# Kernel optimization log

Hardware: AMD Instinct MI355X
Metric: run time of the kernel (lower is better)

Reference implementation:

```python
import jax, jax.numpy as jnp
import numpy as np

B, T = 32, 2048
Q_DIM, K_DIM, V_DIM, A_DIM = 512, 512, 512, 128
TEMP = 1.0


def setup_inputs() -> dict:
    key = jax.random.key(0)
    ks = jax.random.split(key, 8)
    return {
        "query": jax.random.normal(ks[0], (B, Q_DIM), dtype=jnp.float32),
        "keys": jax.random.normal(ks[1], (B, T, K_DIM), dtype=jnp.float32),
        "values": jax.random.normal(ks[2], (B, T, V_DIM), dtype=jnp.float32),
        "prev_attention_weights": jax.random.uniform(ks[3], (B, T), dtype=jnp.float32),
        "mask": jnp.ones((B, T), dtype=jnp.int32),
        # learned params (nn.Linear weight is [out,in]; store as [in,out])
        "Wq": jax.random.normal(ks[4], (Q_DIM, A_DIM), dtype=jnp.float32) * 0.02,
        "Wk": jax.random.normal(ks[5], (K_DIM, A_DIM), dtype=jnp.float32) * 0.02,
        "We": jax.random.normal(ks[6], (A_DIM, 1), dtype=jnp.float32) * 0.02,
    }


def reference(query, keys, values, prev_attention_weights, mask, Wq, Wk, We):
    # additive attention energies
    qp = query @ Wq                                   # [B, A]
    kp = jnp.einsum('btk,ka->bta', keys, Wk)          # [B, T, A]
    energy = jnp.squeeze(jnp.tanh(kp + qp[:, None, :]) @ We, -1)  # [B, T]
    energy = jnp.where(mask == 0, -jnp.inf, energy)
    raw = jax.nn.softmax(energy / TEMP, axis=1)
    # forward attention: fw[0]=raw[0]; fw[t]=(prev[t-1]+prev[t])*raw[t] for t>=1
    prev = prev_attention_weights
    prev_shift = jnp.pad(prev[:, :-1], ((0, 0), (1, 0)))  # prev[t-1], zero at t=0
    fw = raw * (prev + prev_shift)
    fw = fw.at[:, 0].set(raw[:, 0])
    fw = fw / (fw.sum(axis=1, keepdims=True) + 1e-8)
    context = jnp.einsum('bt,btd->bd', fw, values)    # [B, V_DIM]
    return context, fw
```

## Files before the change

### kernel.cpp

```cpp
#include <hip/hip_runtime.h>
#include <cstdint>
#include <cstddef>


#define T_ 2048
#define KD 512
#define AD 128

typedef __attribute__((ext_vector_type(8))) short bf16x8;
typedef __attribute__((ext_vector_type(4))) float f32x4;

__device__ __forceinline__ unsigned pack2bf(float a, float b) {
    unsigned ua = __float_as_uint(a), ub = __float_as_uint(b);
    ua += 0x7FFFu + ((ua >> 16) & 1u);
    ub += 0x7FFFu + ((ub >> 16) & 1u);
    return (ua >> 16) | (ub & 0xFFFF0000u);
}

__global__ __launch_bounds__(256) void prep_kernel(
    const float* __restrict__ query, const float* __restrict__ Wq,
    const float* __restrict__ Wk, float* __restrict__ qp,
    unsigned short* __restrict__ WkT)
{
    __shared__ float sq[128];
    const int tid = threadIdx.x;
    if (blockIdx.x < 32) {
        const int b = blockIdx.x;
        const int a = tid & 127, half = tid >> 7;
        const float* q = query + (size_t)b * KD + half * 256;
        const float* w = Wq + (size_t)(half * 256) * AD + a;
        float s0 = 0.f, s1 = 0.f, s2 = 0.f, s3 = 0.f;
        #pragma unroll 4
        for (int k = 0; k < 256; k += 4) {
            s0 += q[k + 0] * w[(size_t)(k + 0) * AD];
            s1 += q[k + 1] * w[(size_t)(k + 1) * AD];
            s2 += q[k + 2] * w[(size_t)(k + 2) * AD];
            s3 += q[k + 3] * w[(size_t)(k + 3) * AD];
        }
        float s = (s0 + s1) + (s2 + s3);
        if (half == 0) sq[a] = s;
        __syncthreads();
        if (half == 1) qp[(size_t)b * AD + a] = sq[a] + s;
    } else {
        const int blk2 = blockIdx.x - 32;
        const int n = tid & 127, kr = tid >> 7;
        #pragma unroll
        for (int kk = 0; kk < 8; kk++) {
            int k = blk2 * 16 + kr * 8 + kk;
            float v = Wk[(size_t)k * AD + n];
            unsigned u = __float_as_uint(v);
            u += 0x7FFFu + ((u >> 16) & 1u);
            WkT[(size_t)n * KD + k] = (unsigned short)(u >> 16);
        }
    }
}

__global__ __launch_bounds__(256, 2) void energy_kernel(
    const float* __restrict__ keys, const unsigned short* __restrict__ WkT,
    const float* __restrict__ qp, const float* __restrict__ We,
    float* __restrict__ energy)
{
    __shared__ __align__(16) unsigned short sA[128 * 40];
    __shared__ __align__(16) unsigned short sB[128 * 40];
    const int tid = threadIdx.x;
    const int m0 = blockIdx.x * 128;
    const int b = m0 >> 11;

    const int row = tid >> 1, half = tid & 1;
    const float* gA = keys + (size_t)(m0 + row) * KD + half * 16;
    const unsigned short* gB = WkT + (size_t)row * KD + half * 16;
    unsigned short* dA = &sA[row * 40 + half * 16];
    unsigned short* dB = &sB[row * 40 + half * 16];

    const int lane = tid & 63, wv = tid >> 6;
    const int lr = lane & 15, quad = lane >> 4;

    f32x4 acc[2][8];
    #pragma unroll
    for (int mt = 0; mt < 2; mt++)
        #pragma unroll
        for (int nt = 0; nt < 8; nt++)
            acc[mt][nt] = (f32x4){0.f, 0.f, 0.f, 0.f};

    for (int k0 = 0; k0 < KD; k0 += 32) {
        float4 f0 = *(const float4*)(gA + k0 + 0);
        float4 f1 = *(const float4*)(gA + k0 + 4);
        float4 f2 = *(const float4*)(gA + k0 + 8);
        float4 f3 = *(const float4*)(gA + k0 + 12);
        uint4 pa0, pa1;
        pa0.x = pack2bf(f0.x, f0.y); pa0.y = pack2bf(f0.z, f0.w);
        pa0.z = pack2bf(f1.x, f1.y); pa0.w = pack2bf(f1.z, f1.w);
        pa1.x = pack2bf(f2.x, f2.y); pa1.y = pack2bf(f2.z, f2.w);
        pa1.z = pack2bf(f3.x, f3.y); pa1.w = pack2bf(f3.z, f3.w);
        uint4 b0 = *(const uint4*)(gB + k0);
        uint4 b1 = *(const uint4*)(gB + k0 + 8);
        ((uint4*)dA)[0] = pa0; ((uint4*)dA)[1] = pa1;
        ((uint4*)dB)[0] = b0;  ((uint4*)dB)[1] = b1;
        __syncthreads();

        bf16x8 af[2], bfm[8];
        #pragma unroll
        for (int mt = 0; mt < 2; mt++)
            af[mt] = *(const bf16x8*)&sA[(wv * 32 + mt * 16 + lr) * 40 + quad * 8];
        #pragma unroll
        for (int nt = 0; nt < 8; nt++)
            bfm[nt] = *(const bf16x8*)&sB[(nt * 16 + lr) * 40 + quad * 8];
        #pragma unroll
        for (int mt = 0; mt < 2; mt++)
            #pragma unroll
            for (int nt = 0; nt < 8; nt++)
                acc[mt][nt] = __builtin_amdgcn_mfma_f32_16x16x32_bf16(
                    af[mt], bfm[nt], acc[mt][nt], 0, 0, 0);
        __syncthreads();
    }

    float part[2][4] = {{0.f, 0.f, 0.f, 0.f}, {0.f, 0.f, 0.f, 0.f}};
    #pragma unroll
    for (int nt = 0; nt < 8; nt++) {
        int col = nt * 16 + lr;
        float we = We[col];
        float q  = qp[(size_t)b * AD + col];
        #pragma unroll
        for (int mt = 0; mt < 2; mt++)
            #pragma unroll
            for (int r = 0; r < 4; r++) {
                float x = acc[mt][nt][r] + q;
                float e2 = __expf(2.0f * x);
                float th = 1.0f - 2.0f / (e2 + 1.0f);
                part[mt][r] += we * th;
            }
    }
    #pragma unroll
    for (int mt = 0; mt < 2; mt++)
        #pragma unroll
        for (int r = 0; r < 4; r++) {
            float v = part[mt][r];
            v += __shfl_xor(v, 1); v += __shfl_xor(v, 2);
            v += __shfl_xor(v, 4); v += __shfl_xor(v, 8);
            if (lr == 0)
                energy[(size_t)m0 + wv * 32 + mt * 16 + quad * 4 + r] = v;
        }
}

__device__ __forceinline__ float block_red_max(float v, float* sred) {
    #pragma unroll
    for (int m = 1; m < 64; m <<= 1) v = fmaxf(v, __shfl_xor(v, m));
    if ((threadIdx.x & 63) == 0) sred[threadIdx.x >> 6] = v;
    __syncthreads();
    float r = fmaxf(fmaxf(sred[0], sred[1]), fmaxf(sred[2], sred[3]));
    __syncthreads();
    return r;
}
__device__ __forceinline__ float block_red_sum(float v, float* sred) {
    #pragma unroll
    for (int m = 1; m < 64; m <<= 1) v += __shfl_xor(v, m);
    if ((threadIdx.x & 63) == 0) sred[threadIdx.x >> 6] = v;
    __syncthreads();
    float r = (sred[0] + sred[1]) + (sred[2] + sred[3]);
    __syncthreads();
    return r;
}

__global__ __launch_bounds__(256) void ctx_fused_kernel(
    const float* __restrict__ energy, const float* __restrict__ prev,
    const int* __restrict__ mask, const float* __restrict__ values,
    float* __restrict__ fw, float* __restrict__ part)
{
    __shared__ float sred[4];
    __shared__ float sfw[2048];
    __shared__ float4 sacc[128];
    const int b = blockIdx.x >> 4, ts = blockIdx.x & 15;
    const int tid = threadIdx.x;
    const size_t base = (size_t)b * T_;

    float e[8];
    #pragma unroll
    for (int i = 0; i < 8; i++) {
        int t = tid + 256 * i;
        float ev = energy[base + t];
        if (mask[base + t] == 0) ev = -__builtin_inff();
        e[i] = ev;
    }
    float mx = e[0];
    #pragma unroll
    for (int i = 1; i < 8; i++) mx = fmaxf(mx, e[i]);
    mx = block_red_max(mx, sred);

    float ex[8]; float s = 0.f;
    #pragma unroll
    for (int i = 0; i < 8; i++) { ex[i] = __expf(e[i] - mx); s += ex[i]; }
    s = block_red_sum(s, sred);
    const float invS = 1.0f / s;

    float fwv[8]; float s2 = 0.f;
    #pragma unroll
    for (int i = 0; i < 8; i++) {
        int t = tid + 256 * i;
        float pv = prev[base + t];
        float pm = (t == 0) ? 0.f : prev[base + t - 1];
        float r = ex[i] * invS;
        fwv[i] = (t == 0) ? r : r * (pv + pm);
        s2 += fwv[i];
    }
    s2 = block_red_sum(s2, sred);
    const float invD = 1.0f / (s2 + 1e-8f);
    #pragma unroll
    for (int i = 0; i < 8; i++)
        sfw[tid + 256 * i] = fwv[i] * invD;
    __syncthreads();

    const int t0 = ts * 128;
    if (tid < 128) fw[base + t0 + tid] = sfw[t0 + tid];

    const int d4 = tid & 127, tp = tid >> 7;
    const float* sf = &sfw[t0];
    const float4* vp = (const float4*)values + ((size_t)b * T_ + t0 + tp) * 128 + d4;
    float4 acc = {0.f, 0.f, 0.f, 0.f};
    #pragma unroll 8
    for (int i = 0; i < 64; i++) {
        float f = sf[tp + 2 * i];
        float4 v = vp[(size_t)i * 256];
        acc.x += f * v.x; acc.y += f * v.y; acc.z += f * v.z; acc.w += f * v.w;
    }
    if (tp) sacc[d4] = acc;
    __syncthreads();
    if (!tp) {
        float4 o = sacc[d4];
        o.x += acc.x; o.y += acc.y; o.z += acc.z; o.w += acc.w;
        ((float4*)part)[(size_t)blockIdx.x * 128 + d4] = o;
    }
}

__global__ __launch_bounds__(256) void ctx_reduce_kernel(
    const float* __restrict__ part, float* __restrict__ ctx)
{
    const int idx = blockIdx.x * 256 + threadIdx.x;
    const int b = idx >> 9, d = idx & 511;
    float s = 0.f;
    #pragma unroll
    for (int ts = 0; ts < 16; ts++)
        s += part[((size_t)(b * 16 + ts)) * 512 + d];
    ctx[idx] = s;
}

extern "C" void kernel_launch(void* const* d_in, const int* in_sizes, int n_in,
                              void* d_out, int out_size, void* d_ws, size_t ws_size,
                              hipStream_t stream) {
    const float* query  = (const float*)d_in[0];
    const float* keys   = (const float*)d_in[1];
    const float* values = (const float*)d_in[2];
    const float* prev   = (const float*)d_in[3];
    const int*   mask   = (const int*)d_in[4];
    const float* Wq     = (const float*)d_in[5];
    const float* Wk     = (const float*)d_in[6];
    const float* We     = (const float*)d_in[7];

    float* ctx = (float*)d_out;
    float* fw  = ctx + 32 * 512;

    float* wsf = (float*)d_ws;
    float* qp     = wsf;
    float* part   = wsf + 4096;
    float* energy = wsf + 4096 + 262144;
    unsigned short* WkT = (unsigned short*)(wsf + 4096 + 262144 + 65536);

    prep_kernel<<<dim3(64), dim3(256), 0, stream>>>(query, Wq, Wk, qp, WkT);
    energy_kernel<<<dim3(512), dim3(256), 0, stream>>>(keys, WkT, qp, We, energy);
    ctx_fused_kernel<<<dim3(512), dim3(256), 0, stream>>>(energy, prev, mask, values, fw, part);
    ctx_reduce_kernel<<<dim3(64), dim3(256), 0, stream>>>(part, ctx);
}
```

Baseline: 310.9 us.

## Load MFMA fragments directly from global memory and prefetch values before softmax

The energy GEMM no longer stages keys and WkT through LDS. Each wave loads its own A and B fragments straight from global memory into registers, which removes the shared-memory round trip and both block barriers per k-step. The trade-off is more redundant global/L2 reads of WkT and less coalesced key loads. The context kernel also issues the first eight value loads before the softmax reductions, overlapping their latency with that computation at the cost of extra registers.

```diff
diff --git a/kernel.cpp b/kernel.cpp
--- a/kernel.cpp
+++ b/kernel.cpp
@@ -55,25 +55,20 @@
     }
 }
 
-__global__ __launch_bounds__(256, 2) void energy_kernel(
+__global__ __launch_bounds__(256) void energy_kernel(
     const float* __restrict__ keys, const unsigned short* __restrict__ WkT,
     const float* __restrict__ qp, const float* __restrict__ We,
     float* __restrict__ energy)
 {
-    __shared__ __align__(16) unsigned short sA[128 * 40];
-    __shared__ __align__(16) unsigned short sB[128 * 40];
     const int tid = threadIdx.x;
-    const int m0 = blockIdx.x * 128;
-    const int b = m0 >> 11;
-
-    const int row = tid >> 1, half = tid & 1;
-    const float* gA = keys + (size_t)(m0 + row) * KD + half * 16;
-    const unsigned short* gB = WkT + (size_t)row * KD + half * 16;
-    unsigned short* dA = &sA[row * 40 + half * 16];
-    unsigned short* dB = &sB[row * 40 + half * 16];
-
     const int lane = tid & 63, wv = tid >> 6;
     const int lr = lane & 15, quad = lane >> 4;
+    const int m0 = blockIdx.x * 128 + wv * 32;
+    const int b = (blockIdx.x * 128) >> 11;
+
+    const float* gA0 = keys + (size_t)(m0 + lr) * KD + quad * 8;
+    const float* gA1 = keys + (size_t)(m0 + 16 + lr) * KD + quad * 8;
+    const unsigned short* gB = WkT + (size_t)lr * KD + quad * 8;
 
     f32x4 acc[2][8];
     #pragma unroll
@@ -82,36 +77,31 @@
         for (int nt = 0; nt < 8; nt++)
             acc[mt][nt] = (f32x4){0.f, 0.f, 0.f, 0.f};
 
+    #pragma unroll 2
     for (int k0 = 0; k0 < KD; k0 += 32) {
-        float4 f0 = *(const float4*)(gA + k0 + 0);
-        float4 f1 = *(const float4*)(gA + k0 + 4);
-        float4 f2 = *(const float4*)(gA + k0 + 8);
-        float4 f3 = *(const float4*)(gA + k0 + 12);
-        uint4 pa0, pa1;
-        pa0.x = pack2bf(f0.x, f0.y); pa0.y = pack2bf(f0.z, f0.w);
-        pa0.z = pack2bf(f1.x, f1.y); pa0.w = pack2bf(f1.z, f1.w);
-        pa1.x = pack2bf(f2.x, f2.y); pa1.y = pack2bf(f2.z, f2.w);
-        pa1.z = pack2bf(f3.x, f3.y); pa1.w = pack2bf(f3.z, f3.w);
-        uint4 b0 = *(const uint4*)(gB + k0);
-        uint4 b1 = *(const uint4*)(gB + k0 + 8);
-        ((uint4*)dA)[0] = pa0; ((uint4*)dA)[1] = pa1;
-        ((uint4*)dB)[0] = b0;  ((uint4*)dB)[1] = b1;
-        __syncthreads();
-
-        bf16x8 af[2], bfm[8];
-        #pragma unroll
-        for (int mt = 0; mt < 2; mt++)
-            af[mt] = *(const bf16x8*)&sA[(wv * 32 + mt * 16 + lr) * 40 + quad * 8];
+        uint4 braw[8];
         #pragma unroll
         for (int nt = 0; nt < 8; nt++)
-            bfm[nt] = *(const bf16x8*)&sB[(nt * 16 + lr) * 40 + quad * 8];
-        #pragma unroll
-        for (int mt = 0; mt < 2; mt++)
-            #pragma unroll
-            for (int nt = 0; nt < 8; nt++)
-                acc[mt][nt] = __builtin_amdgcn_mfma_f32_16x16x32_bf16(
-                    af[mt], bfm[nt], acc[mt][nt], 0, 0, 0);
-        __syncthreads();
+            braw[nt] = *(const uint4*)(gB + (size_t)(nt * 16) * KD + k0);
+        float4 a00 = *(const float4*)(gA0 + k0);
+        float4 a01 = *(const float4*)(gA0 + k0 + 4);
+        float4 a10 = *(const float4*)(gA1 + k0);
+        float4 a11 = *(const float4*)(gA1 + k0 + 4);
+        uint4 p0, p1;
+        p0.x = pack2bf(a00.x, a00.y); p0.y = pack2bf(a00.z, a00.w);
+        p0.z = pack2bf(a01.x, a01.y); p0.w = pack2bf(a01.z, a01.w);
+        p1.x = pack2bf(a10.x, a10.y); p1.y = pack2bf(a10.z, a10.w);
+        p1.z = pack2bf(a11.x, a11.y); p1.w = pack2bf(a11.z, a11.w);
+        bf16x8 af0, af1;
+        __builtin_memcpy(&af0, &p0, 16);
+        __builtin_memcpy(&af1, &p1, 16);
+        #pragma unroll
+        for (int nt = 0; nt < 8; nt++) {
+            bf16x8 bf;
+            __builtin_memcpy(&bf, &braw[nt], 16);
+            acc[0][nt] = __builtin_amdgcn_mfma_f32_16x16x32_bf16(af0, bf, acc[0][nt], 0, 0, 0);
+            acc[1][nt] = __builtin_amdgcn_mfma_f32_16x16x32_bf16(af1, bf, acc[1][nt], 0, 0, 0);
+        }
     }
 
     float part[2][4] = {{0.f, 0.f, 0.f, 0.f}, {0.f, 0.f, 0.f, 0.f}};
@@ -138,7 +128,7 @@
             v += __shfl_xor(v, 1); v += __shfl_xor(v, 2);
             v += __shfl_xor(v, 4); v += __shfl_xor(v, 8);
             if (lr == 0)
-                energy[(size_t)m0 + wv * 32 + mt * 16 + quad * 4 + r] = v;
+                energy[(size_t)m0 + mt * 16 + quad * 4 + r] = v;
         }
 }
 
@@ -172,6 +162,13 @@
     const int b = blockIdx.x >> 4, ts = blockIdx.x & 15;
     const int tid = threadIdx.x;
     const size_t base = (size_t)b * T_;
+    const int t0 = ts * 128;
+
+    const int d4 = tid & 127, tp = tid >> 7;
+    const float4* vp = (const float4*)values + ((size_t)b * T_ + t0 + tp) * 128 + d4;
+    float4 pre[8];
+    #pragma unroll
+    for (int i = 0; i < 8; i++) pre[i] = vp[(size_t)i * 256];
 
     float e[8];
     #pragma unroll
@@ -209,15 +206,18 @@
         sfw[tid + 256 * i] = fwv[i] * invD;
     __syncthreads();
 
-    const int t0 = ts * 128;
     if (tid < 128) fw[base + t0 + tid] = sfw[t0 + tid];
 
-    const int d4 = tid & 127, tp = tid >> 7;
     const float* sf = &sfw[t0];
-    const float4* vp = (const float4*)values + ((size_t)b * T_ + t0 + tp) * 128 + d4;
     float4 acc = {0.f, 0.f, 0.f, 0.f};
+    #pragma unroll
+    for (int i = 0; i < 8; i++) {
+        float f = sf[tp + 2 * i];
+        float4 v = pre[i];
+        acc.x += f * v.x; acc.y += f * v.y; acc.z += f * v.z; acc.w += f * v.w;
+    }
     #pragma unroll 8
-    for (int i = 0; i < 64; i++) {
+    for (int i = 8; i < 64; i++) {
         float f = sf[tp + 2 * i];
         float4 v = vp[(size_t)i * 256];
         acc.x += f * v.x; acc.y += f * v.y; acc.z += f * v.z; acc.w += f * v.w;
```

After: 318.6 us. 2.5% more time.

## Double-buffer LDS tiles in energy GEMM and prefetch values before softmax

Applied to the files above, without the earlier changes.

The energy kernel now uses double-buffered shared-memory tiles. Each iteration issues the global loads for the next K slice before running the MFMAs on the current slice, then converts and stores that next slice into the alternate buffer, which halves the barriers per iteration. The context kernel issues its first eight value loads at kernel entry so they overlap with the softmax and forward-attention reductions. The cost is double the LDS footprint and extra registers for the prefetched data, which may lower occupancy.

```diff
diff --git a/kernel.cpp b/kernel.cpp
--- a/kernel.cpp
+++ b/kernel.cpp
@@ -60,8 +60,8 @@
     const float* __restrict__ qp, const float* __restrict__ We,
     float* __restrict__ energy)
 {
-    __shared__ __align__(16) unsigned short sA[128 * 40];
-    __shared__ __align__(16) unsigned short sB[128 * 40];
+    __shared__ __align__(16) unsigned short sA[2][128 * 40];
+    __shared__ __align__(16) unsigned short sB[2][128 * 40];
     const int tid = threadIdx.x;
     const int m0 = blockIdx.x * 128;
     const int b = m0 >> 11;
@@ -69,8 +69,7 @@
     const int row = tid >> 1, half = tid & 1;
     const float* gA = keys + (size_t)(m0 + row) * KD + half * 16;
     const unsigned short* gB = WkT + (size_t)row * KD + half * 16;
-    unsigned short* dA = &sA[row * 40 + half * 16];
-    unsigned short* dB = &sB[row * 40 + half * 16];
+    const int doff = row * 40 + half * 16;
 
     const int lane = tid & 63, wv = tid >> 6;
     const int lr = lane & 15, quad = lane >> 4;
@@ -82,36 +81,60 @@
         for (int nt = 0; nt < 8; nt++)
             acc[mt][nt] = (f32x4){0.f, 0.f, 0.f, 0.f};
 
-    for (int k0 = 0; k0 < KD; k0 += 32) {
-        float4 f0 = *(const float4*)(gA + k0 + 0);
-        float4 f1 = *(const float4*)(gA + k0 + 4);
-        float4 f2 = *(const float4*)(gA + k0 + 8);
-        float4 f3 = *(const float4*)(gA + k0 + 12);
+    {
+        float4 f0 = *(const float4*)(gA + 0);
+        float4 f1 = *(const float4*)(gA + 4);
+        float4 f2 = *(const float4*)(gA + 8);
+        float4 f3 = *(const float4*)(gA + 12);
+        uint4 b0 = *(const uint4*)(gB + 0);
+        uint4 b1 = *(const uint4*)(gB + 8);
         uint4 pa0, pa1;
         pa0.x = pack2bf(f0.x, f0.y); pa0.y = pack2bf(f0.z, f0.w);
         pa0.z = pack2bf(f1.x, f1.y); pa0.w = pack2bf(f1.z, f1.w);
         pa1.x = pack2bf(f2.x, f2.y); pa1.y = pack2bf(f2.z, f2.w);
         pa1.z = pack2bf(f3.x, f3.y); pa1.w = pack2bf(f3.z, f3.w);
-        uint4 b0 = *(const uint4*)(gB + k0);
-        uint4 b1 = *(const uint4*)(gB + k0 + 8);
-        ((uint4*)dA)[0] = pa0; ((uint4*)dA)[1] = pa1;
-        ((uint4*)dB)[0] = b0;  ((uint4*)dB)[1] = b1;
-        __syncthreads();
-
+        ((uint4*)&sA[0][doff])[0] = pa0; ((uint4*)&sA[0][doff])[1] = pa1;
+        ((uint4*)&sB[0][doff])[0] = b0;  ((uint4*)&sB[0][doff])[1] = b1;
+    }
+    __syncthreads();
+
+    int cur = 0;
+    for (int k0 = 0; k0 < KD; k0 += 32) {
+        const int kn = k0 + 32;
+        const bool has_next = kn < KD;
+        float4 f0, f1, f2, f3; uint4 bb0, bb1;
+        if (has_next) {
+            f0 = *(const float4*)(gA + kn + 0);
+            f1 = *(const float4*)(gA + kn + 4);
+            f2 = *(const float4*)(gA + kn + 8);
+            f3 = *(const float4*)(gA + kn + 12);
+            bb0 = *(const uint4*)(gB + kn);
+            bb1 = *(const uint4*)(gB + kn + 8);
+        }
         bf16x8 af[2], bfm[8];
         #pragma unroll
         for (int mt = 0; mt < 2; mt++)
-            af[mt] = *(const bf16x8*)&sA[(wv * 32 + mt * 16 + lr) * 40 + quad * 8];
+            af[mt] = *(const bf16x8*)&sA[cur][(wv * 32 + mt * 16 + lr) * 40 + quad * 8];
         #pragma unroll
         for (int nt = 0; nt < 8; nt++)
-            bfm[nt] = *(const bf16x8*)&sB[(nt * 16 + lr) * 40 + quad * 8];
+            bfm[nt] = *(const bf16x8*)&sB[cur][(nt * 16 + lr) * 40 + quad * 8];
         #pragma unroll
         for (int mt = 0; mt < 2; mt++)
             #pragma unroll
             for (int nt = 0; nt < 8; nt++)
                 acc[mt][nt] = __builtin_amdgcn_mfma_f32_16x16x32_bf16(
                     af[mt], bfm[nt], acc[mt][nt], 0, 0, 0);
+        if (has_next) {
+            uint4 pa0, pa1;
+            pa0.x = pack2bf(f0.x, f0.y); pa0.y = pack2bf(f0.z, f0.w);
+            pa0.z = pack2bf(f1.x, f1.y); pa0.w = pack2bf(f1.z, f1.w);
+            pa1.x = pack2bf(f2.x, f2.y); pa1.y = pack2bf(f2.z, f2.w);
+            pa1.z = pack2bf(f3.x, f3.y); pa1.w = pack2bf(f3.z, f3.w);
+            ((uint4*)&sA[cur ^ 1][doff])[0] = pa0; ((uint4*)&sA[cur ^ 1][doff])[1] = pa1;
+            ((uint4*)&sB[cur ^ 1][doff])[0] = bb0; ((uint4*)&sB[cur ^ 1][doff])[1] = bb1;
+        }
         __syncthreads();
+        cur ^= 1;
     }
 
     float part[2][4] = {{0.f, 0.f, 0.f, 0.f}, {0.f, 0.f, 0.f, 0.f}};
@@ -172,6 +195,13 @@
     const int b = blockIdx.x >> 4, ts = blockIdx.x & 15;
     const int tid = threadIdx.x;
     const size_t base = (size_t)b * T_;
+    const int t0 = ts * 128;
+
+    const int d4 = tid & 127, tp = tid >> 7;
+    const float4* vp = (const float4*)values + ((size_t)b * T_ + t0 + tp) * 128 + d4;
+    float4 pre[8];
+    #pragma unroll
+    for (int i = 0; i < 8; i++) pre[i] = vp[(size_t)i * 256];
 
     float e[8];
     #pragma unroll
@@ -209,15 +239,18 @@
         sfw[tid + 256 * i] = fwv[i] * invD;
     __syncthreads();
 
-    const int t0 = ts * 128;
     if (tid < 128) fw[base + t0 + tid] = sfw[t0 + tid];
 
-    const int d4 = tid & 127, tp = tid >> 7;
     const float* sf = &sfw[t0];
-    const float4* vp = (const float4*)values + ((size_t)b * T_ + t0 + tp) * 128 + d4;
     float4 acc = {0.f, 0.f, 0.f, 0.f};
+    #pragma unroll
+    for (int i = 0; i < 8; i++) {
+        float f = sf[tp + 2 * i];
+        float4 v = pre[i];
+        acc.x += f * v.x; acc.y += f * v.y; acc.z += f * v.z; acc.w += f * v.w;
+    }
     #pragma unroll 8
-    for (int i = 0; i < 64; i++) {
+    for (int i = 8; i < 64; i++) {
         float f = sf[tp + 2 * i];
         float4 v = vp[(size_t)i * 256];
         acc.x += f * v.x; acc.y += f * v.y; acc.z += f * v.z; acc.w += f * v.w;
```

Measured after the change: 308.3 us. No clear change (-0.8%).
